# Kernel optimization log

Measured on AMD Instinct MI355X. Metric: run time of the kernel, lower is better.

## Reference

```python
import jax, jax.numpy as jnp
import numpy as np

N_NODES = 100000
N_EDGES = 400000
N_REL = 3
N_LAYERS = 2
D = 128          # input feature dim == hidden_dim so weights stack cleanly
N_CLASSES = 2


def setup_inputs() -> dict:
    key = jax.random.key(0)
    ks = jax.random.split(key, 7)
    x = jax.random.normal(ks[0], (N_NODES, D), dtype=jnp.float32)
    edge_index = jax.random.randint(ks[1], (N_REL, 2, N_EDGES), 0, N_NODES, dtype=jnp.int32)
    # SAGEConv params per (layer, relation): neighbor weight, root weight, bias
    Wn = jax.random.normal(ks[2], (N_LAYERS, N_REL, D, D), dtype=jnp.float32) * (1.0 / np.sqrt(D))
    Wr = jax.random.normal(ks[3], (N_LAYERS, N_REL, D, D), dtype=jnp.float32) * (1.0 / np.sqrt(D))
    b = jax.random.normal(ks[4], (N_LAYERS, N_REL, D), dtype=jnp.float32) * 0.02
    Wc = jax.random.normal(ks[5], (D, N_CLASSES), dtype=jnp.float32) * (1.0 / np.sqrt(D))
    bc = jax.random.normal(ks[6], (N_CLASSES,), dtype=jnp.float32) * 0.02
    return {"x": x, "edge_index": edge_index, "Wn": Wn, "Wr": Wr, "b": b, "Wc": Wc, "bc": bc}


def _mean_agg(h, ei, n_nodes):
    # gather source features, scatter-mean into destination nodes
    src, dst = ei[0], ei[1]
    s = jax.ops.segment_sum(h[src], dst, num_segments=n_nodes)          # [N, D]
    cnt = jax.ops.segment_sum(jnp.ones((ei.shape[1],), h.dtype), dst, num_segments=n_nodes)
    return s / jnp.maximum(cnt, 1.0)[:, None]


def reference(x, edge_index, Wn, Wr, b, Wc, bc):
    n = x.shape[0]
    h = x
    L, R = Wn.shape[0], Wn.shape[1]
    for l in range(L):
        out = jnp.zeros((n, Wn.shape[-1]), h.dtype)
        for r in range(R):
            # SAGEConv: lin_l(mean neighbors) + lin_r(root) + bias; HeteroConv sums relations
            agg = _mean_agg(h, edge_index[r], n)
            out = out + agg @ Wn[l, r] + h @ Wr[l, r] + b[l, r]
        h = jax.nn.relu(out) if l < L - 1 else out  # dropout is eval-mode identity
    return h @ Wc + bc
```

## Files before the change

kernel.cpp:

```cpp
#include <hip/hip_runtime.h>

#define NN 100000
#define NE 400000
#define NR 3
#define DD 128
#define NROWS (NR * NN)
#define NEDGES (NR * NE)
#define SCAN_BLOCKS ((NROWS + 1023) / 1024)

typedef float f32x4 __attribute__((ext_vector_type(4)));
typedef __bf16 bf16x8 __attribute__((ext_vector_type(8)));

__device__ __forceinline__ unsigned short f2bf(float f) {
    unsigned int u = __float_as_uint(f);
    u += 0x7fff + ((u >> 16) & 1);
    return (unsigned short)(u >> 16);
}

__device__ __forceinline__ void gload16(const void* g, void* l) {
    __builtin_amdgcn_global_load_lds(
        (const __attribute__((address_space(1))) void*)g,
        (__attribute__((address_space(3))) void*)l, 16, 0, 0);
}

__global__ __launch_bounds__(256) void cvt_x(const float* __restrict__ x,
                                             unsigned short* __restrict__ xb) {
    int i = blockIdx.x * 256 + threadIdx.x;
    const float4* xf = reinterpret_cast<const float4*>(x + (size_t)i * 8);
    float4 a = xf[0], b = xf[1];
    uint4 o;
    o.x = (unsigned)f2bf(a.x) | ((unsigned)f2bf(a.y) << 16);
    o.y = (unsigned)f2bf(a.z) | ((unsigned)f2bf(a.w) << 16);
    o.z = (unsigned)f2bf(b.x) | ((unsigned)f2bf(b.y) << 16);
    o.w = (unsigned)f2bf(b.z) | ((unsigned)f2bf(b.w) << 16);
    reinterpret_cast<uint4*>(xb)[i] = o;
}

__global__ __launch_bounds__(256) void prep_w(const float* __restrict__ Wn,
                                              const float* __restrict__ Wr,
                                              unsigned short* __restrict__ Wt) {
    int t = blockIdx.x * 256 + threadIdx.x;
    if (t >= 2 * 128 * 512) return;
    int l = t >> 16;
    int rem = t & 65535;
    int n = rem >> 9;
    int k = rem & 511;
    int rk = k >> 7, kk = k & 127;
    float v;
    if (rk < 3) {
        v = Wn[(((size_t)l * 3 + rk) * 128 + kk) * 128 + n];
    } else {
        const float* WrL = Wr + (size_t)l * 3 * 128 * 128;
        v = WrL[kk * 128 + n] + WrL[128 * 128 + kk * 128 + n] + WrL[2 * 128 * 128 + kk * 128 + n];
    }
    Wt[((size_t)l * 128 + n) * 512 + k] = f2bf(v);
}

__global__ __launch_bounds__(256) void prep_b(const float* __restrict__ b,
                                              float* __restrict__ bias) {
    int t = threadIdx.x;
    int l = t >> 7, n = t & 127;
    bias[t] = b[l * 384 + n] + b[l * 384 + 128 + n] + b[l * 384 + 256 + n];
}

__global__ __launch_bounds__(256) void csr_count(const int* __restrict__ ei,
                                                 int* __restrict__ cnt) {
    int t = blockIdx.x * 256 + threadIdx.x;
    if (t >= NEDGES) return;
    int r = t / NE;
    int e = t - r * NE;
    int dst = ei[(r * 2 + 1) * NE + e];
    atomicAdd(&cnt[r * NN + dst], 1);
}

__global__ __launch_bounds__(256) void scan1(const int* __restrict__ cnt,
                                             int* __restrict__ row_start,
                                             int* __restrict__ bsum) {
    __shared__ int sh[256];
    int b0 = blockIdx.x * 1024;
    int t = threadIdx.x;
    int v[4];
    int s = 0;
    #pragma unroll
    for (int j = 0; j < 4; ++j) {
        int idx = b0 + t * 4 + j;
        v[j] = (idx < NROWS) ? cnt[idx] : 0;
        s += v[j];
    }
    sh[t] = s;
    __syncthreads();
    for (int off = 1; off < 256; off <<= 1) {
        int val = (t >= off) ? sh[t - off] : 0;
        __syncthreads();
        sh[t] += val;
        __syncthreads();
    }
    int excl = (t == 0) ? 0 : sh[t - 1];
    if (t == 255) bsum[blockIdx.x] = sh[255];
    #pragma unroll
    for (int j = 0; j < 4; ++j) {
        int idx = b0 + t * 4 + j;
        if (idx < NROWS) { row_start[idx] = excl; excl += v[j]; }
    }
}

__global__ __launch_bounds__(512) void scan2(int* __restrict__ bsum, int nb) {
    __shared__ int sh[512];
    int t = threadIdx.x;
    sh[t] = (t < nb) ? bsum[t] : 0;
    __syncthreads();
    for (int off = 1; off < 512; off <<= 1) {
        int val = (t >= off) ? sh[t - off] : 0;
        __syncthreads();
        sh[t] += val;
        __syncthreads();
    }
    int excl = (t == 0) ? 0 : sh[t - 1];
    if (t < nb) bsum[t] = excl;
}

__global__ __launch_bounds__(256) void scan3(int* __restrict__ row_start,
                                             const int* __restrict__ bsum) {
    int idx = blockIdx.x * 256 + threadIdx.x;
    if (idx < NROWS) row_start[idx] += bsum[idx >> 10];
}

__global__ __launch_bounds__(256) void csr_fill(const int* __restrict__ ei,
                                                const int* __restrict__ row_start,
                                                int* __restrict__ cursor,
                                                int* __restrict__ bucket) {
    int t = blockIdx.x * 256 + threadIdx.x;
    if (t >= NEDGES) return;
    int r = t / NE;
    int e = t - r * NE;
    int src = ei[(r * 2 + 0) * NE + e];
    int dst = ei[(r * 2 + 1) * NE + e];
    int i = r * NN + dst;
    int pos = row_start[i] + atomicAdd(&cursor[i], 1);
    bucket[pos] = src;
}

__global__ __launch_bounds__(256) void gnn_gather(const unsigned short* __restrict__ h,
                                                  const int* __restrict__ bucket,
                                                  const int* __restrict__ row_start,
                                                  const int* __restrict__ cnt,
                                                  unsigned short* __restrict__ agg) {
    int wid = (blockIdx.x * 256 + threadIdx.x) >> 6;
    int lane = threadIdx.x & 63;
    if (wid >= NROWS) return;
    int base = row_start[wid];
    int deg = cnt[wid];
    const unsigned int* hw = reinterpret_cast<const unsigned int*>(h);
    float a0 = 0.f, a1 = 0.f, b0 = 0.f, b1 = 0.f;
    float c0 = 0.f, c1 = 0.f, d0 = 0.f, d1 = 0.f;
    int e = 0;
    for (; e + 4 <= deg; e += 4) {
        int s0 = bucket[base + e + 0];
        int s1 = bucket[base + e + 1];
        int s2 = bucket[base + e + 2];
        int s3 = bucket[base + e + 3];
        unsigned int v0 = hw[(size_t)s0 * 64 + lane];
        unsigned int v1 = hw[(size_t)s1 * 64 + lane];
        unsigned int v2 = hw[(size_t)s2 * 64 + lane];
        unsigned int v3 = hw[(size_t)s3 * 64 + lane];
        a0 += __uint_as_float(v0 << 16); a1 += __uint_as_float(v0 & 0xffff0000u);
        b0 += __uint_as_float(v1 << 16); b1 += __uint_as_float(v1 & 0xffff0000u);
        c0 += __uint_as_float(v2 << 16); c1 += __uint_as_float(v2 & 0xffff0000u);
        d0 += __uint_as_float(v3 << 16); d1 += __uint_as_float(v3 & 0xffff0000u);
    }
    for (; e < deg; ++e) {
        int s0 = bucket[base + e];
        unsigned int v0 = hw[(size_t)s0 * 64 + lane];
        a0 += __uint_as_float(v0 << 16); a1 += __uint_as_float(v0 & 0xffff0000u);
    }
    a0 = (a0 + b0) + (c0 + d0);
    a1 = (a1 + b1) + (c1 + d1);
    float sc = (deg > 0) ? (1.0f / (float)deg) : 0.0f;
    a0 *= sc; a1 *= sc;
    unsigned int o = (unsigned)f2bf(a0) | ((unsigned)f2bf(a1) << 16);
    reinterpret_cast<unsigned int*>(agg + (size_t)wid * DD)[lane] = o;
}

template <int RELU>
__global__ __launch_bounds__(256) void gemm_mfma(
    const unsigned short* __restrict__ aggb,
    const unsigned short* __restrict__ hb,
    const unsigned short* __restrict__ Wt,
    const float* __restrict__ bias,
    unsigned short* __restrict__ outb)
{
    __shared__ __align__(16) unsigned short As[2 * 128 * 32];
    __shared__ __align__(16) unsigned short Bs[2 * 128 * 32];
    const int t = threadIdx.x;
    const int w = t >> 6, lane = t & 63;
    const int m0 = blockIdx.x * 128;
    const int wr = w >> 1, wc = w & 1;
    const int fr = lane & 15;
    const int fq = lane >> 4;
    f32x4 acc[4][4] = {};

    auto stage = [&](int s, int buf) {
        const int srcid = s >> 2;
        const int k0 = (s & 3) * 32;
        const unsigned short* Asrc = (srcid < 3) ? (aggb + (size_t)srcid * NN * DD) : hb;
        #pragma unroll
        for (int i = 0; i < 2; ++i) {
            int row = i * 64 + w * 16 + (lane >> 2);
            int grow = m0 + row;
            if (grow > NN - 1) grow = NN - 1;
            const unsigned short* gA = Asrc + (size_t)grow * DD + k0 + (lane & 3) * 8;
            gload16(gA, (char*)As + buf * 8192 + i * 4096 + w * 1024);
            const unsigned short* gB = Wt + (size_t)row * 512 + srcid * 128 + k0 + (lane & 3) * 8;
            gload16(gB, (char*)Bs + buf * 8192 + i * 4096 + w * 1024);
        }
    };

    stage(0, 0);
    #pragma unroll
    for (int s = 0; s < 16; ++s) {
        const int cur = s & 1;
        __syncthreads();
        if (s + 1 < 16) stage(s + 1, cur ^ 1);
        bf16x8 af[4], bfr[4];
        #pragma unroll
        for (int m = 0; m < 4; ++m)
            af[m] = *reinterpret_cast<const bf16x8*>(As + cur * 4096 + (wr * 64 + m * 16 + fr) * 32 + fq * 8);
        #pragma unroll
        for (int n = 0; n < 4; ++n)
            bfr[n] = *reinterpret_cast<const bf16x8*>(Bs + cur * 4096 + (wc * 64 + n * 16 + fr) * 32 + fq * 8);
        #pragma unroll
        for (int m = 0; m < 4; ++m)
            #pragma unroll
            for (int n = 0; n < 4; ++n)
                acc[m][n] = __builtin_amdgcn_mfma_f32_16x16x32_bf16(af[m], bfr[n], acc[m][n], 0, 0, 0);
    }

    #pragma unroll
    for (int n = 0; n < 4; ++n) {
        int col = wc * 64 + n * 16 + fr;
        float bs = bias[col];
        #pragma unroll
        for (int m = 0; m < 4; ++m) {
            int rbase = m0 + wr * 64 + m * 16 + fq * 4;
            #pragma unroll
            for (int j = 0; j < 4; ++j) {
                int row = rbase + j;
                if (row < NN) {
                    float v = acc[m][n][j] + bs;
                    if (RELU) v = fmaxf(v, 0.f);
                    outb[(size_t)row * DD + col] = f2bf(v);
                }
            }
        }
    }
}

__global__ __launch_bounds__(256) void classify(const unsigned short* __restrict__ h2,
                                                const float* __restrict__ Wc,
                                                const float* __restrict__ bc,
                                                float* __restrict__ out) {
    int wid = (blockIdx.x * 256 + threadIdx.x) >> 6;
    int lane = threadIdx.x & 63;
    if (wid >= NN) return;
    float4 wc4 = reinterpret_cast<const float4*>(Wc)[lane];
    unsigned int v = reinterpret_cast<const unsigned int*>(h2 + (size_t)wid * DD)[lane];
    float v0 = __uint_as_float(v << 16);
    float v1 = __uint_as_float(v & 0xffff0000u);
    float p0 = v0 * wc4.x + v1 * wc4.z;
    float p1 = v0 * wc4.y + v1 * wc4.w;
    #pragma unroll
    for (int off = 1; off < 64; off <<= 1) {
        p0 += __shfl_xor(p0, off);
        p1 += __shfl_xor(p1, off);
    }
    if (lane == 0) {
        out[(size_t)wid * 2 + 0] = p0 + bc[0];
        out[(size_t)wid * 2 + 1] = p1 + bc[1];
    }
}

extern "C" void kernel_launch(void* const* d_in, const int* in_sizes, int n_in,
                              void* d_out, int out_size, void* d_ws, size_t ws_size,
                              hipStream_t stream) {
    const float* x  = (const float*)d_in[0];
    const int*   ei = (const int*)d_in[1];
    const float* Wn = (const float*)d_in[2];
    const float* Wr = (const float*)d_in[3];
    const float* b  = (const float*)d_in[4];
    const float* Wc = (const float*)d_in[5];
    const float* bc = (const float*)d_in[6];
    float* out = (float*)d_out;

    char* p = (char*)d_ws;
    unsigned short* aggb = (unsigned short*)p;  p += (size_t)NR * NN * DD * 2;
    unsigned short* xb   = (unsigned short*)p;  p += (size_t)NN * DD * 2;
    unsigned short* h1b  = (unsigned short*)p;  p += (size_t)NN * DD * 2;
    unsigned short* h2b  = (unsigned short*)p;  p += (size_t)NN * DD * 2;
    unsigned short* Wt   = (unsigned short*)p;  p += (size_t)2 * 128 * 512 * 2;
    float* bias          = (float*)p;           p += 2 * 128 * 4;
    int* bucket          = (int*)p;             p += (size_t)NEDGES * 4;
    int* cnt             = (int*)p;             p += (size_t)NROWS * 4;
    int* row_start       = (int*)p;             p += (size_t)NROWS * 4;
    int* cursor          = (int*)p;             p += (size_t)NROWS * 4;
    int* bsum            = (int*)p;             p += 512 * 4;

    hipMemsetAsync(cnt, 0, NROWS * sizeof(int), stream);
    hipMemsetAsync(cursor, 0, NROWS * sizeof(int), stream);

    csr_count<<<(NEDGES + 255) / 256, 256, 0, stream>>>(ei, cnt);
    scan1<<<SCAN_BLOCKS, 256, 0, stream>>>(cnt, row_start, bsum);
    scan2<<<1, 512, 0, stream>>>(bsum, SCAN_BLOCKS);
    scan3<<<(NROWS + 255) / 256, 256, 0, stream>>>(row_start, bsum);
    csr_fill<<<(NEDGES + 255) / 256, 256, 0, stream>>>(ei, row_start, cursor, bucket);

    cvt_x<<<(NN * DD / 8 + 255) / 256, 256, 0, stream>>>(x, xb);
    prep_w<<<(2 * 128 * 512 + 255) / 256, 256, 0, stream>>>(Wn, Wr, Wt);
    prep_b<<<1, 256, 0, stream>>>(b, bias);

    const int gatherBlocks = (NROWS * 64) / 256;
    const int gemmBlocks = (NN + 127) / 128;

    gnn_gather<<<gatherBlocks, 256, 0, stream>>>(xb, bucket, row_start, cnt, aggb);
    gemm_mfma<1><<<gemmBlocks, 256, 0, stream>>>(aggb, xb, Wt, bias, h1b);

    gnn_gather<<<gatherBlocks, 256, 0, stream>>>(h1b, bucket, row_start, cnt, aggb);
    gemm_mfma<0><<<gemmBlocks, 256, 0, stream>>>(aggb, h1b, Wt + (size_t)128 * 512,
                                                 bias + 128, h2b);

    classify<<<(NN * 64 + 255) / 256, 256, 0, stream>>>(h2b, Wc, bc, out);
}
```

Measured before the change: 518.2 us.

## Transform before aggregating, fuse gather with bias/relu/classifier, merge prep kernels

Applies linearity of mean aggregation: each layer first runs one GEMM that projects h into four 128-wide slices (three neighbor projections and the summed root projection), then a fused gather averages the projected neighbor rows per relation, adds root and bias, applies relu or the final classifier. This replaces the 3xN aggregated-feature buffer and the separate classify kernel, and cuts the GEMM K dimension from 512 to 128. It also merges the x conversion, weight, bias and zeroing work into one prep kernel, folds scan3 into its consumers, pre-shifts bucket indices into byte offsets, and adds an LDS swizzle. In exchange, gathered rows are read from a 1 KB-strided Y buffer and rounding happens after the projection.

```diff
diff --git a/kernel.cpp b/kernel.cpp
--- a/kernel.cpp
+++ b/kernel.cpp
@@ -23,44 +23,51 @@
         (__attribute__((address_space(3))) void*)l, 16, 0, 0);
 }
 
-__global__ __launch_bounds__(256) void cvt_x(const float* __restrict__ x,
-                                             unsigned short* __restrict__ xb) {
-    int i = blockIdx.x * 256 + threadIdx.x;
-    const float4* xf = reinterpret_cast<const float4*>(x + (size_t)i * 8);
-    float4 a = xf[0], b = xf[1];
-    uint4 o;
-    o.x = (unsigned)f2bf(a.x) | ((unsigned)f2bf(a.y) << 16);
-    o.y = (unsigned)f2bf(a.z) | ((unsigned)f2bf(a.w) << 16);
-    o.z = (unsigned)f2bf(b.x) | ((unsigned)f2bf(b.y) << 16);
-    o.w = (unsigned)f2bf(b.z) | ((unsigned)f2bf(b.w) << 16);
-    reinterpret_cast<uint4*>(xb)[i] = o;
-}
-
-__global__ __launch_bounds__(256) void prep_w(const float* __restrict__ Wn,
-                                              const float* __restrict__ Wr,
-                                              unsigned short* __restrict__ Wt) {
-    int t = blockIdx.x * 256 + threadIdx.x;
-    if (t >= 2 * 128 * 512) return;
-    int l = t >> 16;
-    int rem = t & 65535;
-    int n = rem >> 9;
-    int k = rem & 511;
-    int rk = k >> 7, kk = k & 127;
-    float v;
-    if (rk < 3) {
-        v = Wn[(((size_t)l * 3 + rk) * 128 + kk) * 128 + n];
+#define NB_CVT 6250
+#define NB_WT 512
+#define NB_ZERO 586
+__global__ __launch_bounds__(256) void prep_all(const float* __restrict__ x,
+                                                const float* __restrict__ Wn,
+                                                const float* __restrict__ Wr,
+                                                const float* __restrict__ b,
+                                                unsigned short* __restrict__ xb,
+                                                unsigned short* __restrict__ Wt2,
+                                                float* __restrict__ bias,
+                                                unsigned int* __restrict__ zbase) {
+    int bid = blockIdx.x;
+    int tid = threadIdx.x;
+    if (bid < NB_CVT) {
+        int i = bid * 256 + tid;
+        const float4* xf = reinterpret_cast<const float4*>(x + (size_t)i * 8);
+        float4 a = xf[0], bv = xf[1];
+        uint4 o;
+        o.x = (unsigned)f2bf(a.x) | ((unsigned)f2bf(a.y) << 16);
+        o.y = (unsigned)f2bf(a.z) | ((unsigned)f2bf(a.w) << 16);
+        o.z = (unsigned)f2bf(bv.x) | ((unsigned)f2bf(bv.y) << 16);
+        o.w = (unsigned)f2bf(bv.z) | ((unsigned)f2bf(bv.w) << 16);
+        reinterpret_cast<uint4*>(xb)[i] = o;
+    } else if (bid < NB_CVT + NB_WT) {
+        int t = (bid - NB_CVT) * 256 + tid;
+        int l = t >> 16;
+        int rem = t & 65535;
+        int n512 = rem >> 7;
+        int kk = rem & 127;
+        int rk = n512 >> 7, n = n512 & 127;
+        float v;
+        if (rk < 3) {
+            v = Wn[(((size_t)l * 3 + rk) * 128 + kk) * 128 + n];
+        } else {
+            const float* WrL = Wr + (size_t)l * 3 * 128 * 128;
+            v = WrL[kk * 128 + n] + WrL[128 * 128 + kk * 128 + n] + WrL[2 * 128 * 128 + kk * 128 + n];
+        }
+        Wt2[t] = f2bf(v);
+    } else if (bid == NB_CVT + NB_WT) {
+        int l = tid >> 7, n = tid & 127;
+        bias[tid] = b[l * 384 + n] + b[l * 384 + 128 + n] + b[l * 384 + 256 + n];
     } else {
-        const float* WrL = Wr + (size_t)l * 3 * 128 * 128;
-        v = WrL[kk * 128 + n] + WrL[128 * 128 + kk * 128 + n] + WrL[2 * 128 * 128 + kk * 128 + n];
-    }
-    Wt[((size_t)l * 128 + n) * 512 + k] = f2bf(v);
-}
-
-__global__ __launch_bounds__(256) void prep_b(const float* __restrict__ b,
-                                              float* __restrict__ bias) {
-    int t = threadIdx.x;
-    int l = t >> 7, n = t & 127;
-    bias[t] = b[l * 384 + n] + b[l * 384 + 128 + n] + b[l * 384 + 256 + n];
+        int i = (bid - NB_CVT - NB_WT - 1) * 256 + tid;
+        if (i < 150000) reinterpret_cast<uint4*>(zbase)[i] = make_uint4(0, 0, 0, 0);
+    }
 }
 
 __global__ __launch_bounds__(256) void csr_count(const int* __restrict__ ei,
@@ -119,14 +126,9 @@
     if (t < nb) bsum[t] = excl;
 }
 
-__global__ __launch_bounds__(256) void scan3(int* __restrict__ row_start,
-                                             const int* __restrict__ bsum) {
-    int idx = blockIdx.x * 256 + threadIdx.x;
-    if (idx < NROWS) row_start[idx] += bsum[idx >> 10];
-}
-
 __global__ __launch_bounds__(256) void csr_fill(const int* __restrict__ ei,
                                                 const int* __restrict__ row_start,
+                                                const int* __restrict__ bsum,
                                                 int* __restrict__ cursor,
                                                 int* __restrict__ bucket) {
     int t = blockIdx.x * 256 + threadIdx.x;
@@ -136,98 +138,59 @@
     int src = ei[(r * 2 + 0) * NE + e];
     int dst = ei[(r * 2 + 1) * NE + e];
     int i = r * NN + dst;
-    int pos = row_start[i] + atomicAdd(&cursor[i], 1);
-    bucket[pos] = src;
-}
-
-__global__ __launch_bounds__(256) void gnn_gather(const unsigned short* __restrict__ h,
-                                                  const int* __restrict__ bucket,
-                                                  const int* __restrict__ row_start,
-                                                  const int* __restrict__ cnt,
-                                                  unsigned short* __restrict__ agg) {
-    int wid = (blockIdx.x * 256 + threadIdx.x) >> 6;
-    int lane = threadIdx.x & 63;
-    if (wid >= NROWS) return;
-    int base = row_start[wid];
-    int deg = cnt[wid];
-    const unsigned int* hw = reinterpret_cast<const unsigned int*>(h);
-    float a0 = 0.f, a1 = 0.f, b0 = 0.f, b1 = 0.f;
-    float c0 = 0.f, c1 = 0.f, d0 = 0.f, d1 = 0.f;
-    int e = 0;
-    for (; e + 4 <= deg; e += 4) {
-        int s0 = bucket[base + e + 0];
-        int s1 = bucket[base + e + 1];
-        int s2 = bucket[base + e + 2];
-        int s3 = bucket[base + e + 3];
-        unsigned int v0 = hw[(size_t)s0 * 64 + lane];
-        unsigned int v1 = hw[(size_t)s1 * 64 + lane];
-        unsigned int v2 = hw[(size_t)s2 * 64 + lane];
-        unsigned int v3 = hw[(size_t)s3 * 64 + lane];
-        a0 += __uint_as_float(v0 << 16); a1 += __uint_as_float(v0 & 0xffff0000u);
-        b0 += __uint_as_float(v1 << 16); b1 += __uint_as_float(v1 & 0xffff0000u);
-        c0 += __uint_as_float(v2 << 16); c1 += __uint_as_float(v2 & 0xffff0000u);
-        d0 += __uint_as_float(v3 << 16); d1 += __uint_as_float(v3 & 0xffff0000u);
-    }
-    for (; e < deg; ++e) {
-        int s0 = bucket[base + e];
-        unsigned int v0 = hw[(size_t)s0 * 64 + lane];
-        a0 += __uint_as_float(v0 << 16); a1 += __uint_as_float(v0 & 0xffff0000u);
-    }
-    a0 = (a0 + b0) + (c0 + d0);
-    a1 = (a1 + b1) + (c1 + d1);
-    float sc = (deg > 0) ? (1.0f / (float)deg) : 0.0f;
-    a0 *= sc; a1 *= sc;
-    unsigned int o = (unsigned)f2bf(a0) | ((unsigned)f2bf(a1) << 16);
-    reinterpret_cast<unsigned int*>(agg + (size_t)wid * DD)[lane] = o;
-}
-
-template <int RELU>
-__global__ __launch_bounds__(256) void gemm_mfma(
-    const unsigned short* __restrict__ aggb,
-    const unsigned short* __restrict__ hb,
-    const unsigned short* __restrict__ Wt,
-    const float* __restrict__ bias,
-    unsigned short* __restrict__ outb)
+    int pos = row_start[i] + bsum[i >> 10] + atomicAdd(&cursor[i], 1);
+    bucket[pos] = src << 10;
+}
+
+__global__ __launch_bounds__(256) void gemm_y(
+    const unsigned short* __restrict__ Ab,
+    const unsigned short* __restrict__ WtL,
+    unsigned short* __restrict__ Yb)
 {
     __shared__ __align__(16) unsigned short As[2 * 128 * 32];
     __shared__ __align__(16) unsigned short Bs[2 * 128 * 32];
     const int t = threadIdx.x;
     const int w = t >> 6, lane = t & 63;
-    const int m0 = blockIdx.x * 128;
-    const int wr = w >> 1, wc = w & 1;
+    const int bid = blockIdx.x;
+    const int p = bid & 3;
+    const int m0 = (bid >> 2) * 128;
+    const unsigned short* WtP = WtL + p * 128 * 128;
+    const int wr = w >> 1, wcol = w & 1;
     const int fr = lane & 15;
     const int fq = lane >> 4;
+    const int gsw = (((lane & 3) ^ ((lane >> 2) & 3) ^ ((lane >> 4) & 3))) * 8;
+    const int rsw = (fq ^ ((fr ^ (fr >> 2)) & 3)) * 8;
     f32x4 acc[4][4] = {};
 
     auto stage = [&](int s, int buf) {
-        const int srcid = s >> 2;
-        const int k0 = (s & 3) * 32;
-        const unsigned short* Asrc = (srcid < 3) ? (aggb + (size_t)srcid * NN * DD) : hb;
+        const int k0 = s * 32;
         #pragma unroll
         for (int i = 0; i < 2; ++i) {
             int row = i * 64 + w * 16 + (lane >> 2);
             int grow = m0 + row;
             if (grow > NN - 1) grow = NN - 1;
-            const unsigned short* gA = Asrc + (size_t)grow * DD + k0 + (lane & 3) * 8;
+            const unsigned short* gA = Ab + (size_t)grow * DD + k0 + gsw;
             gload16(gA, (char*)As + buf * 8192 + i * 4096 + w * 1024);
-            const unsigned short* gB = Wt + (size_t)row * 512 + srcid * 128 + k0 + (lane & 3) * 8;
+            const unsigned short* gB = WtP + (size_t)row * 128 + k0 + gsw;
             gload16(gB, (char*)Bs + buf * 8192 + i * 4096 + w * 1024);
         }
     };
 
     stage(0, 0);
     #pragma unroll
-    for (int s = 0; s < 16; ++s) {
+    for (int s = 0; s < 4; ++s) {
         const int cur = s & 1;
         __syncthreads();
-        if (s + 1 < 16) stage(s + 1, cur ^ 1);
+        if (s + 1 < 4) stage(s + 1, cur ^ 1);
+        const unsigned short* As_c = As + cur * 4096;
+        const unsigned short* Bs_c = Bs + cur * 4096;
         bf16x8 af[4], bfr[4];
         #pragma unroll
         for (int m = 0; m < 4; ++m)
-            af[m] = *reinterpret_cast<const bf16x8*>(As + cur * 4096 + (wr * 64 + m * 16 + fr) * 32 + fq * 8);
+            af[m] = *reinterpret_cast<const bf16x8*>(As_c + (wr * 64 + m * 16 + fr) * 32 + rsw);
         #pragma unroll
         for (int n = 0; n < 4; ++n)
-            bfr[n] = *reinterpret_cast<const bf16x8*>(Bs + cur * 4096 + (wc * 64 + n * 16 + fr) * 32 + fq * 8);
+            bfr[n] = *reinterpret_cast<const bf16x8*>(Bs_c + (wcol * 64 + n * 16 + fr) * 32 + rsw);
         #pragma unroll
         for (int m = 0; m < 4; ++m)
             #pragma unroll
@@ -237,45 +200,95 @@
 
     #pragma unroll
     for (int n = 0; n < 4; ++n) {
-        int col = wc * 64 + n * 16 + fr;
-        float bs = bias[col];
+        int col = p * 128 + wcol * 64 + n * 16 + fr;
         #pragma unroll
         for (int m = 0; m < 4; ++m) {
             int rbase = m0 + wr * 64 + m * 16 + fq * 4;
             #pragma unroll
             for (int j = 0; j < 4; ++j) {
                 int row = rbase + j;
-                if (row < NN) {
-                    float v = acc[m][n][j] + bs;
-                    if (RELU) v = fmaxf(v, 0.f);
-                    outb[(size_t)row * DD + col] = f2bf(v);
-                }
+                if (row < NN) Yb[(size_t)row * 512 + col] = f2bf(acc[m][n][j]);
             }
         }
     }
 }
 
-__global__ __launch_bounds__(256) void classify(const unsigned short* __restrict__ h2,
-                                                const float* __restrict__ Wc,
-                                                const float* __restrict__ bc,
-                                                float* __restrict__ out) {
+template <int FINAL>
+__global__ __launch_bounds__(256) void gather_fused(
+    const unsigned short* __restrict__ Yb,
+    const int* __restrict__ bucket,
+    const int* __restrict__ row_start,
+    const int* __restrict__ bsum,
+    const int* __restrict__ cnt,
+    const float* __restrict__ biasL,
+    const float* __restrict__ Wc,
+    const float* __restrict__ bc,
+    unsigned short* __restrict__ hout,
+    float* __restrict__ out)
+{
     int wid = (blockIdx.x * 256 + threadIdx.x) >> 6;
     int lane = threadIdx.x & 63;
     if (wid >= NN) return;
-    float4 wc4 = reinterpret_cast<const float4*>(Wc)[lane];
-    unsigned int v = reinterpret_cast<const unsigned int*>(h2 + (size_t)wid * DD)[lane];
-    float v0 = __uint_as_float(v << 16);
-    float v1 = __uint_as_float(v & 0xffff0000u);
-    float p0 = v0 * wc4.x + v1 * wc4.z;
-    float p1 = v0 * wc4.y + v1 * wc4.w;
-    #pragma unroll
-    for (int off = 1; off < 64; off <<= 1) {
-        p0 += __shfl_xor(p0, off);
-        p1 += __shfl_xor(p1, off);
-    }
-    if (lane == 0) {
-        out[(size_t)wid * 2 + 0] = p0 + bc[0];
-        out[(size_t)wid * 2 + 1] = p1 + bc[1];
+    const char* Yc = (const char*)Yb;
+    const unsigned int lo = lane * 4u;
+    unsigned int rootv = *(const unsigned int*)(Yc + (size_t)wid * 1024u + 768u + lo);
+    float t0 = __uint_as_float(rootv << 16);
+    float t1 = __uint_as_float(rootv & 0xffff0000u);
+    #pragma unroll
+    for (int r = 0; r < 3; ++r) {
+        int id = r * NN + wid;
+        int base = row_start[id] + bsum[id >> 10];
+        int deg = cnt[id];
+        unsigned int rb = r * 256u + lo;
+        float a0 = 0.f, a1 = 0.f, b0 = 0.f, b1 = 0.f;
+        float c0 = 0.f, c1 = 0.f, d0 = 0.f, d1 = 0.f;
+        int e = 0;
+        for (; e + 4 <= deg; e += 4) {
+            unsigned int o0 = (unsigned)bucket[base + e + 0] + rb;
+            unsigned int o1 = (unsigned)bucket[base + e + 1] + rb;
+            unsigned int o2 = (unsigned)bucket[base + e + 2] + rb;
+            unsigned int o3 = (unsigned)bucket[base + e + 3] + rb;
+            unsigned int v0 = *(const unsigned int*)(Yc + o0);
+            unsigned int v1 = *(const unsigned int*)(Yc + o1);
+            unsigned int v2 = *(const unsigned int*)(Yc + o2);
+            unsigned int v3 = *(const unsigned int*)(Yc + o3);
+            a0 += __uint_as_float(v0 << 16); a1 += __uint_as_float(v0 & 0xffff0000u);
+            b0 += __uint_as_float(v1 << 16); b1 += __uint_as_float(v1 & 0xffff0000u);
+            c0 += __uint_as_float(v2 << 16); c1 += __uint_as_float(v2 & 0xffff0000u);
+            d0 += __uint_as_float(v3 << 16); d1 += __uint_as_float(v3 & 0xffff0000u);
+        }
+        for (; e < deg; ++e) {
+            unsigned int o0 = (unsigned)bucket[base + e] + rb;
+            unsigned int v0 = *(const unsigned int*)(Yc + o0);
+            a0 += __uint_as_float(v0 << 16); a1 += __uint_as_float(v0 & 0xffff0000u);
+        }
+        float s0 = (a0 + b0) + (c0 + d0);
+        float s1 = (a1 + b1) + (c1 + d1);
+        float iv = (deg > 0) ? (1.0f / (float)deg) : 0.0f;
+        t0 = fmaf(s0, iv, t0);
+        t1 = fmaf(s1, iv, t1);
+    }
+    float2 bb = reinterpret_cast<const float2*>(biasL)[lane];
+    t0 += bb.x;
+    t1 += bb.y;
+    if (!FINAL) {
+        t0 = fmaxf(t0, 0.f);
+        t1 = fmaxf(t1, 0.f);
+        unsigned int o = (unsigned)f2bf(t0) | ((unsigned)f2bf(t1) << 16);
+        reinterpret_cast<unsigned int*>(hout)[wid * 64 + lane] = o;
+    } else {
+        float4 w4 = reinterpret_cast<const float4*>(Wc)[lane];
+        float p0 = t0 * w4.x + t1 * w4.z;
+        float p1 = t0 * w4.y + t1 * w4.w;
+        #pragma unroll
+        for (int off = 1; off < 64; off <<= 1) {
+            p0 += __shfl_xor(p0, off);
+            p1 += __shfl_xor(p1, off);
+        }
+        if (lane == 0) {
+            out[(size_t)wid * 2 + 0] = p0 + bc[0];
+            out[(size_t)wid * 2 + 1] = p1 + bc[1];
+        }
     }
 }
 
@@ -292,40 +305,33 @@
     float* out = (float*)d_out;
 
     char* p = (char*)d_ws;
-    unsigned short* aggb = (unsigned short*)p;  p += (size_t)NR * NN * DD * 2;
-    unsigned short* xb   = (unsigned short*)p;  p += (size_t)NN * DD * 2;
-    unsigned short* h1b  = (unsigned short*)p;  p += (size_t)NN * DD * 2;
-    unsigned short* h2b  = (unsigned short*)p;  p += (size_t)NN * DD * 2;
-    unsigned short* Wt   = (unsigned short*)p;  p += (size_t)2 * 128 * 512 * 2;
-    float* bias          = (float*)p;           p += 2 * 128 * 4;
-    int* bucket          = (int*)p;             p += (size_t)NEDGES * 4;
-    int* cnt             = (int*)p;             p += (size_t)NROWS * 4;
-    int* row_start       = (int*)p;             p += (size_t)NROWS * 4;
-    int* cursor          = (int*)p;             p += (size_t)NROWS * 4;
-    int* bsum            = (int*)p;             p += 512 * 4;
-
-    hipMemsetAsync(cnt, 0, NROWS * sizeof(int), stream);
-    hipMemsetAsync(cursor, 0, NROWS * sizeof(int), stream);
+    unsigned short* Yb  = (unsigned short*)p;  p += (size_t)NN * 512 * 2;
+    unsigned short* xb  = (unsigned short*)p;  p += (size_t)NN * DD * 2;
+    unsigned short* h1b = (unsigned short*)p;  p += (size_t)NN * DD * 2;
+    unsigned short* Wt2 = (unsigned short*)p;  p += (size_t)2 * 4 * 128 * 128 * 2;
+    float* bias         = (float*)p;           p += 2 * 128 * 4;
+    int* bucket         = (int*)p;             p += (size_t)NEDGES * 4;
+    int* row_start      = (int*)p;             p += (size_t)NROWS * 4;
+    int* bsum           = (int*)p;             p += 512 * 4;
+    int* cnt            = (int*)p;             p += (size_t)NROWS * 4;
+    int* cursor         = (int*)p;             p += (size_t)NROWS * 4;
+
+    prep_all<<<NB_CVT + NB_WT + 1 + NB_ZERO, 256, 0, stream>>>(
+        x, Wn, Wr, b, xb, Wt2, bias, (unsigned int*)cnt);
 
     csr_count<<<(NEDGES + 255) / 256, 256, 0, stream>>>(ei, cnt);
     scan1<<<SCAN_BLOCKS, 256, 0, stream>>>(cnt, row_start, bsum);
     scan2<<<1, 512, 0, stream>>>(bsum, SCAN_BLOCKS);
-    scan3<<<(NROWS + 255) / 256, 256, 0, stream>>>(row_start, bsum);
-    csr_fill<<<(NEDGES + 255) / 256, 256, 0, stream>>>(ei, row_start, cursor, bucket);
-
-    cvt_x<<<(NN * DD / 8 + 255) / 256, 256, 0, stream>>>(x, xb);
-    prep_w<<<(2 * 128 * 512 + 255) / 256, 256, 0, stream>>>(Wn, Wr, Wt);
-    prep_b<<<1, 256, 0, stream>>>(b, bias);
-
-    const int gatherBlocks = (NROWS * 64) / 256;
-    const int gemmBlocks = (NN + 127) / 128;
-
-    gnn_gather<<<gatherBlocks, 256, 0, stream>>>(xb, bucket, row_start, cnt, aggb);
-    gemm_mfma<1><<<gemmBlocks, 256, 0, stream>>>(aggb, xb, Wt, bias, h1b);
-
-    gnn_gather<<<gatherBlocks, 256, 0, stream>>>(h1b, bucket, row_start, cnt, aggb);
-    gemm_mfma<0><<<gemmBlocks, 256, 0, stream>>>(aggb, h1b, Wt + (size_t)128 * 512,
-                                                 bias + 128, h2b);
-
-    classify<<<(NN * 64 + 255) / 256, 256, 0, stream>>>(h2b, Wc, bc, out);
-}
+    csr_fill<<<(NEDGES + 255) / 256, 256, 0, stream>>>(ei, row_start, bsum, cursor, bucket);
+
+    const int gemmBlocks = ((NN + 127) / 128) * 4;
+    const int gatherBlocks = NN * 64 / 256;
+
+    gemm_y<<<gemmBlocks, 256, 0, stream>>>(xb, Wt2, Yb);
+    gather_fused<0><<<gatherBlocks, 256, 0, stream>>>(Yb, bucket, row_start, bsum, cnt,
+                                                      bias, nullptr, nullptr, h1b, nullptr);
+
+    gemm_y<<<gemmBlocks, 256, 0, stream>>>(h1b, Wt2 + (size_t)4 * 128 * 128, Yb);
+    gather_fused<1><<<gatherBlocks, 256, 0, stream>>>(Yb, bucket, row_start, bsum, cnt,
+                                                      bias + 128, Wc, bc, nullptr, out);
+}
```

Result: faster. 485.4 us (-6.3%).
